# Kernel optimization log

Hardware: AMD Instinct MI355X
Metric: run time of the kernel (lower is better)

The kernel has to match this reference:

```python
import jax, jax.numpy as jnp
import numpy as np

N_NODES = 10000
N_GRAPHS = 64
IN_DIM = 256
HID = 256
N_CLASSES = 10
N_EDGES = 320000


def _gcn_conv(x, W, b, src, dst):
    # PyG GCNConv: h = x @ W; add self-loops (weight 1); symmetric norm D^-1/2 (A+I) D^-1/2; aggregate; + b
    N = x.shape[0]
    h = x @ W  # [N, H]
    loops = jnp.arange(N, dtype=src.dtype)
    s = jnp.concatenate([src, loops])
    d = jnp.concatenate([dst, loops])
    w = jnp.ones(s.shape[0], dtype=x.dtype)
    deg = jax.ops.segment_sum(w, d, num_segments=N)
    dinv = jnp.where(deg > 0, jax.lax.rsqrt(jnp.maximum(deg, 1.0)), 0.0)
    norm = dinv[s] * dinv[d]  # [E+N]
    msg = h[s] * norm[:, None]  # gather + scale
    out = jax.ops.segment_sum(msg, d, num_segments=N)  # scatter-add
    return out + b


def setup_inputs() -> dict:
    key = jax.random.key(0)
    ks = jax.random.split(key, 12)
    x = jax.random.normal(ks[0], (N_NODES, IN_DIM), dtype=jnp.float32)
    edge_index = jax.random.randint(ks[1], (2, N_EDGES), 0, N_NODES, dtype=jnp.int64)
    batch = jnp.sort(jax.random.randint(ks[2], (N_NODES,), 0, N_GRAPHS, dtype=jnp.int64))
    g = 1.0 / np.sqrt(IN_DIM)
    W1 = jax.random.uniform(ks[3], (IN_DIM, HID), jnp.float32, -g, g)
    b1 = jnp.zeros((HID,), jnp.float32)
    gh = 1.0 / np.sqrt(HID)
    W2 = jax.random.uniform(ks[4], (HID, HID), jnp.float32, -gh, gh)
    b2 = jnp.zeros((HID,), jnp.float32)
    W3 = jax.random.uniform(ks[5], (HID, HID), jnp.float32, -gh, gh)
    b3 = jnp.zeros((HID,), jnp.float32)
    Wlin = jax.random.uniform(ks[6], (HID, N_CLASSES), jnp.float32, -gh, gh)
    blin = jax.random.uniform(ks[7], (N_CLASSES,), jnp.float32, -gh, gh)
    return {"x": x, "W1": W1, "b1": b1, "W2": W2, "b2": b2, "W3": W3, "b3": b3,
            "Wlin": Wlin, "blin": blin, "edge_index": edge_index, "batch": batch}


def reference(x, W1, b1, W2, b2, W3, b3, Wlin, blin, edge_index, batch):
    src, dst = edge_index[0], edge_index[1]
    h = jax.nn.relu(_gcn_conv(x, W1, b1, src, dst))
    h = jax.nn.relu(_gcn_conv(h, W2, b2, src, dst))
    h = jax.nn.relu(_gcn_conv(h, W3, b3, src, dst))
    # global mean pool over graphs (dropout is identity in eval mode)
    sums = jax.ops.segment_sum(h, batch, num_segments=N_GRAPHS)  # [G, H]
    cnts = jax.ops.segment_sum(jnp.ones((h.shape[0],), h.dtype), batch, num_segments=N_GRAPHS)
    pooled = sums / jnp.maximum(cnts, 1.0)[:, None]
    logits = pooled @ Wlin + blin
    return jax.nn.log_softmax(logits, axis=-1)
```

## Files before the change

kernel.cpp:

```cpp
#include <hip/hip_runtime.h>
#include <hip/hip_bf16.h>
#include <math.h>

#define HIDDEN 256
#define NCLS 10

typedef __attribute__((ext_vector_type(8))) short short8;
typedef __attribute__((ext_vector_type(4))) float f32x4;

static __device__ __forceinline__ float bf16lo(unsigned u) {
    return __uint_as_float((u & 0xffffu) << 16);
}
static __device__ __forceinline__ float bf16hi(unsigned u) {
    return __uint_as_float(u & 0xffff0000u);
}
static __device__ __forceinline__ unsigned short f2bf(float f) {
    unsigned x = __float_as_uint(f);
    x += 0x7fffu + ((x >> 16) & 1u);
    return (unsigned short)(x >> 16);
}
static __device__ __forceinline__ unsigned pack2(float lo, float hi) {
    return (unsigned)f2bf(lo) | ((unsigned)f2bf(hi) << 16);
}

static __device__ __forceinline__ void fma8(float* acc, uint4 u, float w) {
    acc[0] = fmaf(bf16lo(u.x), w, acc[0]);
    acc[1] = fmaf(bf16hi(u.x), w, acc[1]);
    acc[2] = fmaf(bf16lo(u.y), w, acc[2]);
    acc[3] = fmaf(bf16hi(u.y), w, acc[3]);
    acc[4] = fmaf(bf16lo(u.z), w, acc[4]);
    acc[5] = fmaf(bf16hi(u.z), w, acc[5]);
    acc[6] = fmaf(bf16lo(u.w), w, acc[6]);
    acc[7] = fmaf(bf16hi(u.w), w, acc[7]);
}

__global__ __launch_bounds__(256) void k_count_prep(const int* __restrict__ dst,
                                                    int* __restrict__ ecnt, int E,
                                                    const float* __restrict__ x,
                                                    unsigned* __restrict__ x16,
                                                    const float* __restrict__ W1,
                                                    const float* __restrict__ W2,
                                                    const float* __restrict__ W3,
                                                    short8* __restrict__ P1,
                                                    short8* __restrict__ P2,
                                                    short8* __restrict__ P3,
                                                    int n4, int nbCount, int nb_cvt) {
    const int b = blockIdx.x;
    if (b < nbCount) {
        int e = b * 256 + threadIdx.x;
        if (e < E) atomicAdd(&ecnt[dst[e]], 1);
    } else if (b < nbCount + nb_cvt) {
        int i = (b - nbCount) * 256 + threadIdx.x;
        if (i < n4) {
            float4 v = reinterpret_cast<const float4*>(x)[i];
            uint2 o;
            o.x = pack2(v.x, v.y);
            o.y = pack2(v.z, v.w);
            reinterpret_cast<uint2*>(x16)[i] = o;
        }
    } else {
        int pb = b - nbCount - nb_cvt;
        int which = pb >> 5;
        int id = (pb & 31) * 256 + threadIdx.x;
        const float* W = (which == 0) ? W1 : (which == 1) ? W2 : W3;
        short8* P = (which == 0) ? P1 : (which == 1) ? P2 : P3;
        int l = id & 63;
        int tt = (id >> 6) & 15;
        int s = id >> 10;
        int col = tt * 16 + (l & 15);
        int k0 = s * 32 + (l >> 4) * 8;
        short8 v;
#pragma unroll
        for (int j = 0; j < 8; ++j)
            v[j] = (short)f2bf(W[(size_t)(k0 + j) * HIDDEN + col]);
        P[id] = v;
    }
}

__global__ __launch_bounds__(1024) void k_scan(const int* __restrict__ ecnt,
                                               int* __restrict__ rowstart,
                                               int* __restrict__ cursor,
                                               float* __restrict__ dinv, int N, int E) {
    __shared__ int sums[1024];
    int t = threadIdx.x;
    const int CH = (N + 1023) / 1024;
    int base = t * CH;
    int local = 0;
    for (int i = 0; i < CH; ++i) {
        int idx = base + i;
        if (idx < N) local += ecnt[idx];
    }
    sums[t] = local;
    __syncthreads();
    for (int off = 1; off < 1024; off <<= 1) {
        int v = (t >= off) ? sums[t - off] : 0;
        __syncthreads();
        sums[t] += v;
        __syncthreads();
    }
    int run = (t == 0) ? 0 : sums[t - 1];
    for (int i = 0; i < CH; ++i) {
        int idx = base + i;
        if (idx < N) {
            rowstart[idx] = run;
            cursor[idx] = run;
            dinv[idx] = rsqrtf((float)(ecnt[idx] + 1));
            run += ecnt[idx];
        }
    }
    if (t == 0) rowstart[N] = E;
}

static __device__ __forceinline__ void gemm_body(const unsigned short* __restrict__ A,
                                                 const short8* __restrict__ P,
                                                 unsigned short* __restrict__ C,
                                                 int bx, int by, int tid) {
    const int l = tid & 63;
    const int w = tid >> 6;
    const int g = l >> 4;
    const int r = l & 15;
    const int mwave = bx * 64 + w * 16;
    const int nb = by * 4;

    f32x4 acc[4] = {};
    const unsigned short* arow = A + (size_t)(mwave + r) * HIDDEN;

#pragma unroll
    for (int s = 0; s < 8; ++s) {
        short8 a = *reinterpret_cast<const short8*>(arow + s * 32 + g * 8);
#pragma unroll
        for (int f = 0; f < 4; ++f) {
            short8 bfrag = P[(s * 16 + nb + f) * 64 + l];
            acc[f] = __builtin_amdgcn_mfma_f32_16x16x32_bf16(a, bfrag, acc[f], 0, 0, 0);
        }
    }
#pragma unroll
    for (int f = 0; f < 4; ++f) {
        int col = by * 64 + f * 16 + r;
#pragma unroll
        for (int q = 0; q < 4; ++q) {
            int row = mwave + g * 4 + q;
            C[(size_t)row * HIDDEN + col] = f2bf(acc[f][q]);
        }
    }
}

__global__ __launch_bounds__(256) void k_gemm(const unsigned short* __restrict__ A,
                                              const short8* __restrict__ P,
                                              unsigned short* __restrict__ C) {
    gemm_body(A, P, C, blockIdx.x, blockIdx.y, threadIdx.x);
}

__global__ __launch_bounds__(256) void k_fill_gemm1(const int* __restrict__ src,
                                                    const int* __restrict__ dst,
                                                    const float* __restrict__ dinv,
                                                    int* __restrict__ cursor,
                                                    uint2* __restrict__ csr, int E,
                                                    const unsigned short* __restrict__ A,
                                                    const short8* __restrict__ P,
                                                    unsigned short* __restrict__ C,
                                                    int nbFill) {
    const int b = blockIdx.x;
    if (b < nbFill) {
        int e = b * 256 + threadIdx.x;
        if (e < E) {
            int d = dst[e];
            int s = src[e];
            int pos = atomicAdd(&cursor[d], 1);
            uint2 ent;
            ent.x = (unsigned)s;
            ent.y = __float_as_uint(dinv[s] * dinv[d]);
            csr[pos] = ent;
        }
    } else {
        int gb = b - nbFill;
        gemm_body(A, P, C, gb >> 2, gb & 3, threadIdx.x);
    }
}

__global__ __launch_bounds__(256) void k_agg(const unsigned* __restrict__ H,
                                             const uint2* __restrict__ csr,
                                             const int* __restrict__ rowstart,
                                             const float* __restrict__ dinv,
                                             const float* __restrict__ bias,
                                             unsigned* __restrict__ out, int N) {
    const int n = blockIdx.x * 4 + (threadIdx.x >> 6);
    if (n >= N) return;
    const int l = threadIdx.x & 63;
    const int q = l & 31;
    const int h = l >> 5;
    const uint4* __restrict__ H4 = reinterpret_cast<const uint4*>(H);

    float acc[8] = {0.f, 0.f, 0.f, 0.f, 0.f, 0.f, 0.f, 0.f};
    if (h == 0) {
        const float di = dinv[n];
        fma8(acc, H4[(size_t)n * 32 + q], di * di);
    }

    const int base = rowstart[n];
    const int e1   = rowstart[n + 1];
    const int nfull = (e1 - base) >> 3;
    const uint2* cp = csr + base + 4 * h;

    if (nfull > 0) {
        uint2 dA0 = cp[0], dA1 = cp[1], dA2 = cp[2], dA3 = cp[3];
        uint4 rA0 = H4[(size_t)dA0.x * 32 + q];
        uint4 rA1 = H4[(size_t)dA1.x * 32 + q];
        uint4 rA2 = H4[(size_t)dA2.x * 32 + q];
        uint4 rA3 = H4[(size_t)dA3.x * 32 + q];
        uint2 dB0 = cp[8], dB1 = cp[9], dB2 = cp[10], dB3 = cp[11];
        for (int it = 0; it + 1 < nfull; ++it) {
            cp += 8;
            uint4 rB0 = H4[(size_t)dB0.x * 32 + q];
            uint4 rB1 = H4[(size_t)dB1.x * 32 + q];
            uint4 rB2 = H4[(size_t)dB2.x * 32 + q];
            uint4 rB3 = H4[(size_t)dB3.x * 32 + q];
            uint2 dC0 = cp[8], dC1 = cp[9], dC2 = cp[10], dC3 = cp[11];
            fma8(acc, rA0, __uint_as_float(dA0.y));
            fma8(acc, rA1, __uint_as_float(dA1.y));
            fma8(acc, rA2, __uint_as_float(dA2.y));
            fma8(acc, rA3, __uint_as_float(dA3.y));
            dA0 = dB0; dA1 = dB1; dA2 = dB2; dA3 = dB3;
            dB0 = dC0; dB1 = dC1; dB2 = dC2; dB3 = dC3;
            rA0 = rB0; rA1 = rB1; rA2 = rB2; rA3 = rB3;
        }
        fma8(acc, rA0, __uint_as_float(dA0.y));
        fma8(acc, rA1, __uint_as_float(dA1.y));
        fma8(acc, rA2, __uint_as_float(dA2.y));
        fma8(acc, rA3, __uint_as_float(dA3.y));
    }
    for (int e = base + 8 * nfull + h; e < e1; e += 2) {
        uint2 ed = csr[e];
        fma8(acc, H4[(size_t)ed.x * 32 + q], __uint_as_float(ed.y));
    }

#pragma unroll
    for (int j = 0; j < 8; ++j) acc[j] += __shfl_xor(acc[j], 32);

    if (h == 0) {
        const float4* __restrict__ b4 = reinterpret_cast<const float4*>(bias);
        float4 ba = b4[q * 2];
        float4 bb = b4[q * 2 + 1];
        uint4 o;
        o.x = pack2(fmaxf(acc[0] + ba.x, 0.f), fmaxf(acc[1] + ba.y, 0.f));
        o.y = pack2(fmaxf(acc[2] + ba.z, 0.f), fmaxf(acc[3] + ba.w, 0.f));
        o.z = pack2(fmaxf(acc[4] + bb.x, 0.f), fmaxf(acc[5] + bb.y, 0.f));
        o.w = pack2(fmaxf(acc[6] + bb.z, 0.f), fmaxf(acc[7] + bb.w, 0.f));
        reinterpret_cast<uint4*>(out)[(size_t)n * 32 + q] = o;
    }
}

__device__ __forceinline__ int lower_bound_i(const int* a, int n, int val) {
    int lo = 0, hi = n;
    while (lo < hi) {
        int mid = (lo + hi) >> 1;
        if (a[mid] < val) lo = mid + 1; else hi = mid;
    }
    return lo;
}

__global__ __launch_bounds__(128) void k_pool_part(const unsigned* __restrict__ H,
                                                   const int* __restrict__ batch,
                                                   float* __restrict__ partial, int N) {
    const int g = blockIdx.x;
    const int s = blockIdx.y;
    const int p = threadIdx.x;
    const int lo = lower_bound_i(batch, N, g);
    const int hi = lower_bound_i(batch, N, g + 1);
    float sx = 0.f, sy = 0.f;
    for (int n = lo + s; n < hi; n += 8) {
        unsigned u = H[(size_t)n * 128 + p];
        sx += bf16lo(u);
        sy += bf16hi(u);
    }
    float2 v; v.x = sx; v.y = sy;
    reinterpret_cast<float2*>(partial)[(size_t)(g * 8 + s) * 128 + p] = v;
}

__global__ __launch_bounds__(256) void k_cls(const float* __restrict__ partial,
                                             const int* __restrict__ batch,
                                             const float* __restrict__ Wlin,
                                             const float* __restrict__ blin,
                                             float* __restrict__ out, int N) {
    __shared__ float part[NCLS][HIDDEN];
    const int g = blockIdx.x;
    const int t = threadIdx.x;
    const int lo = lower_bound_i(batch, N, g);
    const int hi = lower_bound_i(batch, N, g + 1);
    float p = 0.f;
#pragma unroll
    for (int s = 0; s < 8; ++s) p += partial[(size_t)(g * 8 + s) * HIDDEN + t];
    p /= fmaxf((float)(hi - lo), 1.f);
#pragma unroll
    for (int c = 0; c < NCLS; ++c) part[c][t] = p * Wlin[(size_t)t * NCLS + c];
    __syncthreads();
    for (int off = 128; off >= 1; off >>= 1) {
        if (t < off) {
#pragma unroll
            for (int c = 0; c < NCLS; ++c) part[c][t] += part[c][t + off];
        }
        __syncthreads();
    }
    if (t == 0) {
        float lg[NCLS];
        float m = -INFINITY;
#pragma unroll
        for (int c = 0; c < NCLS; ++c) {
            lg[c] = part[c][0] + blin[c];
            m = fmaxf(m, lg[c]);
        }
        float se = 0.f;
#pragma unroll
        for (int c = 0; c < NCLS; ++c) se += expf(lg[c] - m);
        float lse = m + logf(se);
#pragma unroll
        for (int c = 0; c < NCLS; ++c) out[(size_t)g * NCLS + c] = lg[c] - lse;
    }
}


extern "C" void kernel_launch(void* const* d_in, const int* in_sizes, int n_in,
                              void* d_out, int out_size, void* d_ws, size_t ws_size,
                              hipStream_t stream) {
    const float* x    = (const float*)d_in[0];
    const float* W1   = (const float*)d_in[1];
    const float* b1   = (const float*)d_in[2];
    const float* W2   = (const float*)d_in[3];
    const float* b2   = (const float*)d_in[4];
    const float* W3   = (const float*)d_in[5];
    const float* b3   = (const float*)d_in[6];
    const float* Wlin = (const float*)d_in[7];
    const float* blin = (const float*)d_in[8];
    const int*   eidx = (const int*)d_in[9];
    const int*   batch= (const int*)d_in[10];
    float* out = (float*)d_out;

    const int N = in_sizes[0] / HIDDEN;
    const int E = in_sizes[9] / 2;
    const int G = out_size / NCLS;
    const int Mp = (N + 63) & ~63;

    const int* src = eidx;
    const int* dst = eidx + E;

    char* base = (char*)d_ws;
    size_t off = 0;
    auto alloc = [&](size_t bytes) -> void* {
        void* p = base + off;
        off = (off + bytes + 255) & ~(size_t)255;
        return p;
    };
    int*      ecnt     = (int*)     alloc((size_t)N * sizeof(int));
    int*      cursor   = (int*)     alloc((size_t)N * sizeof(int));
    float*    dinv     = (float*)   alloc((size_t)N * sizeof(float));
    int*      rowstart = (int*)     alloc((size_t)(N + 1) * sizeof(int));
    uint2*    csr      = (uint2*)   alloc((size_t)(E + 16) * sizeof(uint2));
    unsigned* x16      = (unsigned*)alloc((size_t)Mp * 128 * sizeof(unsigned));
    unsigned* hA       = (unsigned*)alloc((size_t)Mp * 128 * sizeof(unsigned));
    unsigned* hB       = (unsigned*)alloc((size_t)Mp * 128 * sizeof(unsigned));
    short8*   Wp1      = (short8*)  alloc((size_t)8192 * sizeof(short8));
    short8*   Wp2      = (short8*)  alloc((size_t)8192 * sizeof(short8));
    short8*   Wp3      = (short8*)  alloc((size_t)8192 * sizeof(short8));
    float*    partial  = (float*)   alloc((size_t)G * 8 * HIDDEN * sizeof(float));
    (void)ws_size;

    const int nbCount = (E + 255) / 256;
    const int n4 = N * HIDDEN / 4;
    const int nb_cvt = (n4 + 255) / 256;
    hipMemsetAsync(ecnt, 0, (size_t)N * sizeof(int), stream);
    k_count_prep<<<nbCount + nb_cvt + 96, 256, 0, stream>>>(
        dst, ecnt, E, x, x16, W1, W2, W3, Wp1, Wp2, Wp3, n4, nbCount, nb_cvt);
    k_scan<<<1, 1024, 0, stream>>>(ecnt, rowstart, cursor, dinv, N, E);

    const int nbFill = (E + 255) / 256;
    const int gemmBlocks = (Mp / 64) * 4;
    k_fill_gemm1<<<nbFill + gemmBlocks, 256, 0, stream>>>(
        src, dst, dinv, cursor, csr, E,
        (const unsigned short*)x16, Wp1, (unsigned short*)hA, nbFill);

    const dim3 ggrid(Mp / 64, 4);
    const int agg_blocks = (N + 3) / 4;
    k_agg <<<agg_blocks, 256, 0, stream>>>(hA, csr, rowstart, dinv, b1, hB, N);
    k_gemm<<<ggrid, 256, 0, stream>>>((const unsigned short*)hB, Wp2, (unsigned short*)hA);
    k_agg <<<agg_blocks, 256, 0, stream>>>(hA, csr, rowstart, dinv, b2, hB, N);
    k_gemm<<<ggrid, 256, 0, stream>>>((const unsigned short*)hB, Wp3, (unsigned short*)hA);
    k_agg <<<agg_blocks, 256, 0, stream>>>(hA, csr, rowstart, dinv, b3, hB, N);
    k_pool_part<<<dim3(G, 8), 128, 0, stream>>>(hB, batch, partial, N);
    k_cls <<<G, 256, 0, stream>>>(partial, batch, Wlin, blin, out, N);
}
```

Measured before the change: 166.2 us.

## Split feature matrices into two column halves so aggregation covers one half per pass

Node feature buffers are stored as two contiguous 128-column halves instead of row-major 256 columns. The aggregation kernel gains a second grid dimension, one per half, so each wave gathers 256-byte rows with one dword per lane. It also pipelines 8 edges at a time, double-buffered, in place of the previous split-wave uint4 scheme that needed a cross-half shuffle. The goal is a smaller working set per pass for better L2 reuse and no shuffle reduction, at the cost of reading CSR indices twice and using narrower per-lane loads. The GEMM, pool and classifier indexing are updated to match the new layout.

Measured after the change: 204.4 us. 1.23x slower.

```diff
diff --git a/kernel.cpp b/kernel.cpp
--- a/kernel.cpp
+++ b/kernel.cpp
@@ -9,7 +9,7 @@
 typedef __attribute__((ext_vector_type(4))) float f32x4;
 
 static __device__ __forceinline__ float bf16lo(unsigned u) {
-    return __uint_as_float((u & 0xffffu) << 16);
+    return __uint_as_float(u << 16);
 }
 static __device__ __forceinline__ float bf16hi(unsigned u) {
     return __uint_as_float(u & 0xffff0000u);
@@ -23,16 +23,6 @@
     return (unsigned)f2bf(lo) | ((unsigned)f2bf(hi) << 16);
 }
 
-static __device__ __forceinline__ void fma8(float* acc, uint4 u, float w) {
-    acc[0] = fmaf(bf16lo(u.x), w, acc[0]);
-    acc[1] = fmaf(bf16hi(u.x), w, acc[1]);
-    acc[2] = fmaf(bf16lo(u.y), w, acc[2]);
-    acc[3] = fmaf(bf16hi(u.y), w, acc[3]);
-    acc[4] = fmaf(bf16lo(u.z), w, acc[4]);
-    acc[5] = fmaf(bf16hi(u.z), w, acc[5]);
-    acc[6] = fmaf(bf16lo(u.w), w, acc[6]);
-    acc[7] = fmaf(bf16hi(u.w), w, acc[7]);
-}
 
 __global__ __launch_bounds__(256) void k_count_prep(const int* __restrict__ dst,
                                                     int* __restrict__ ecnt, int E,
@@ -44,7 +34,8 @@
                                                     short8* __restrict__ P1,
                                                     short8* __restrict__ P2,
                                                     short8* __restrict__ P3,
-                                                    int n4, int nbCount, int nb_cvt) {
+                                                    int n4, int nbCount, int nb_cvt,
+                                                    int Mp) {
     const int b = blockIdx.x;
     if (b < nbCount) {
         int e = b * 256 + threadIdx.x;
@@ -56,7 +47,11 @@
             uint2 o;
             o.x = pack2(v.x, v.y);
             o.y = pack2(v.z, v.w);
-            reinterpret_cast<uint2*>(x16)[i] = o;
+            int row = i >> 6;
+            int c4  = i & 63;
+            int half = c4 >> 5;
+            size_t idx = (size_t)half * Mp * 32 + (size_t)row * 32 + (c4 & 31);
+            reinterpret_cast<uint2*>(x16)[idx] = o;
         }
     } else {
         int pb = b - nbCount - nb_cvt;
@@ -114,7 +109,7 @@
 static __device__ __forceinline__ void gemm_body(const unsigned short* __restrict__ A,
                                                  const short8* __restrict__ P,
                                                  unsigned short* __restrict__ C,
-                                                 int bx, int by, int tid) {
+                                                 int bx, int by, int tid, int Mp) {
     const int l = tid & 63;
     const int w = tid >> 6;
     const int g = l >> 4;
@@ -123,11 +118,13 @@
     const int nb = by * 4;
 
     f32x4 acc[4] = {};
-    const unsigned short* arow = A + (size_t)(mwave + r) * HIDDEN;
+    const unsigned short* arow0 = A + (size_t)(mwave + r) * 128 + g * 8;
+    const unsigned short* arow1 = arow0 + (size_t)Mp * 128;
 
 #pragma unroll
     for (int s = 0; s < 8; ++s) {
-        short8 a = *reinterpret_cast<const short8*>(arow + s * 32 + g * 8);
+        const unsigned short* ap = (s < 4) ? arow0 : arow1;
+        short8 a = *reinterpret_cast<const short8*>(ap + (s & 3) * 32);
 #pragma unroll
         for (int f = 0; f < 4; ++f) {
             short8 bfrag = P[(s * 16 + nb + f) * 64 + l];
@@ -137,18 +134,19 @@
 #pragma unroll
     for (int f = 0; f < 4; ++f) {
         int col = by * 64 + f * 16 + r;
+        unsigned short* cb = C + (size_t)(col >> 7) * Mp * 128 + (col & 127);
 #pragma unroll
         for (int q = 0; q < 4; ++q) {
             int row = mwave + g * 4 + q;
-            C[(size_t)row * HIDDEN + col] = f2bf(acc[f][q]);
+            cb[(size_t)row * 128] = f2bf(acc[f][q]);
         }
     }
 }
 
 __global__ __launch_bounds__(256) void k_gemm(const unsigned short* __restrict__ A,
                                               const short8* __restrict__ P,
-                                              unsigned short* __restrict__ C) {
-    gemm_body(A, P, C, blockIdx.x, blockIdx.y, threadIdx.x);
+                                              unsigned short* __restrict__ C, int Mp) {
+    gemm_body(A, P, C, blockIdx.x, blockIdx.y, threadIdx.x, Mp);
 }
 
 __global__ __launch_bounds__(256) void k_fill_gemm1(const int* __restrict__ src,
@@ -159,7 +157,7 @@
                                                     const unsigned short* __restrict__ A,
                                                     const short8* __restrict__ P,
                                                     unsigned short* __restrict__ C,
-                                                    int nbFill) {
+                                                    int nbFill, int Mp) {
     const int b = blockIdx.x;
     if (b < nbFill) {
         int e = b * 256 + threadIdx.x;
@@ -174,7 +172,7 @@
         }
     } else {
         int gb = b - nbFill;
-        gemm_body(A, P, C, gb >> 2, gb & 3, threadIdx.x);
+        gemm_body(A, P, C, gb >> 2, gb & 3, threadIdx.x, Mp);
     }
 }
 
@@ -183,71 +181,103 @@
                                              const int* __restrict__ rowstart,
                                              const float* __restrict__ dinv,
                                              const float* __restrict__ bias,
-                                             unsigned* __restrict__ out, int N) {
+                                             unsigned* __restrict__ out, int N, int Mp) {
     const int n = blockIdx.x * 4 + (threadIdx.x >> 6);
     if (n >= N) return;
+    const int p = blockIdx.y;
     const int l = threadIdx.x & 63;
-    const int q = l & 31;
-    const int h = l >> 5;
-    const uint4* __restrict__ H4 = reinterpret_cast<const uint4*>(H);
-
-    float acc[8] = {0.f, 0.f, 0.f, 0.f, 0.f, 0.f, 0.f, 0.f};
-    if (h == 0) {
+    const unsigned* __restrict__ Hh = H + (size_t)p * Mp * 64;
+
+    float ax, ay;
+    {
         const float di = dinv[n];
-        fma8(acc, H4[(size_t)n * 32 + q], di * di);
+        unsigned u = Hh[(size_t)n * 64 + l];
+        ax = bf16lo(u) * (di * di);
+        ay = bf16hi(u) * (di * di);
     }
 
     const int base = rowstart[n];
     const int e1   = rowstart[n + 1];
     const int nfull = (e1 - base) >> 3;
-    const uint2* cp = csr + base + 4 * h;
+    const uint2* cp = csr + base;
 
     if (nfull > 0) {
-        uint2 dA0 = cp[0], dA1 = cp[1], dA2 = cp[2], dA3 = cp[3];
-        uint4 rA0 = H4[(size_t)dA0.x * 32 + q];
-        uint4 rA1 = H4[(size_t)dA1.x * 32 + q];
-        uint4 rA2 = H4[(size_t)dA2.x * 32 + q];
-        uint4 rA3 = H4[(size_t)dA3.x * 32 + q];
-        uint2 dB0 = cp[8], dB1 = cp[9], dB2 = cp[10], dB3 = cp[11];
-        for (int it = 0; it + 1 < nfull; ++it) {
+        uint2 d1[8];
+        unsigned r0[8], r1[8];
+        float w0[8], w1[8];
+        {
+            uint2 d0[8];
+#pragma unroll
+            for (int j = 0; j < 8; ++j) d0[j] = cp[j];
+#pragma unroll
+            for (int j = 0; j < 8; ++j) {
+                r0[j] = Hh[(size_t)d0[j].x * 64 + l];
+                w0[j] = __uint_as_float(d0[j].y);
+            }
+#pragma unroll
+            for (int j = 0; j < 8; ++j) d1[j] = cp[8 + j];
+        }
+        int it = 0;
+        for (; it + 2 < nfull; it += 2) {
+#pragma unroll
+            for (int j = 0; j < 8; ++j) r1[j] = Hh[(size_t)d1[j].x * 64 + l];
+#pragma unroll
+            for (int j = 0; j < 8; ++j) w1[j] = __uint_as_float(d1[j].y);
+#pragma unroll
+            for (int j = 0; j < 8; ++j) d1[j] = cp[16 + j];
+#pragma unroll
+            for (int j = 0; j < 8; ++j) {
+                ax = fmaf(bf16lo(r0[j]), w0[j], ax);
+                ay = fmaf(bf16hi(r0[j]), w0[j], ay);
+            }
             cp += 8;
-            uint4 rB0 = H4[(size_t)dB0.x * 32 + q];
-            uint4 rB1 = H4[(size_t)dB1.x * 32 + q];
-            uint4 rB2 = H4[(size_t)dB2.x * 32 + q];
-            uint4 rB3 = H4[(size_t)dB3.x * 32 + q];
-            uint2 dC0 = cp[8], dC1 = cp[9], dC2 = cp[10], dC3 = cp[11];
-            fma8(acc, rA0, __uint_as_float(dA0.y));
-            fma8(acc, rA1, __uint_as_float(dA1.y));
-            fma8(acc, rA2, __uint_as_float(dA2.y));
-            fma8(acc, rA3, __uint_as_float(dA3.y));
-            dA0 = dB0; dA1 = dB1; dA2 = dB2; dA3 = dB3;
-            dB0 = dC0; dB1 = dC1; dB2 = dC2; dB3 = dC3;
-            rA0 = rB0; rA1 = rB1; rA2 = rB2; rA3 = rB3;
-        }
-        fma8(acc, rA0, __uint_as_float(dA0.y));
-        fma8(acc, rA1, __uint_as_float(dA1.y));
-        fma8(acc, rA2, __uint_as_float(dA2.y));
-        fma8(acc, rA3, __uint_as_float(dA3.y));
-    }
-    for (int e = base + 8 * nfull + h; e < e1; e += 2) {
+#pragma unroll
+            for (int j = 0; j < 8; ++j) r0[j] = Hh[(size_t)d1[j].x * 64 + l];
+#pragma unroll
+            for (int j = 0; j < 8; ++j) w0[j] = __uint_as_float(d1[j].y);
+#pragma unroll
+            for (int j = 0; j < 8; ++j) d1[j] = cp[16 + j];
+#pragma unroll
+            for (int j = 0; j < 8; ++j) {
+                ax = fmaf(bf16lo(r1[j]), w1[j], ax);
+                ay = fmaf(bf16hi(r1[j]), w1[j], ay);
+            }
+            cp += 8;
+        }
+        if (nfull - it == 2) {
+#pragma unroll
+            for (int j = 0; j < 8; ++j) r1[j] = Hh[(size_t)d1[j].x * 64 + l];
+#pragma unroll
+            for (int j = 0; j < 8; ++j) w1[j] = __uint_as_float(d1[j].y);
+#pragma unroll
+            for (int j = 0; j < 8; ++j) {
+                ax = fmaf(bf16lo(r0[j]), w0[j], ax);
+                ay = fmaf(bf16hi(r0[j]), w0[j], ay);
+            }
+#pragma unroll
+            for (int j = 0; j < 8; ++j) {
+                ax = fmaf(bf16lo(r1[j]), w1[j], ax);
+                ay = fmaf(bf16hi(r1[j]), w1[j], ay);
+            }
+        } else {
+#pragma unroll
+            for (int j = 0; j < 8; ++j) {
+                ax = fmaf(bf16lo(r0[j]), w0[j], ax);
+                ay = fmaf(bf16hi(r0[j]), w0[j], ay);
+            }
+        }
+    }
+    for (int e = base + 8 * nfull; e < e1; ++e) {
         uint2 ed = csr[e];
-        fma8(acc, H4[(size_t)ed.x * 32 + q], __uint_as_float(ed.y));
-    }
-
-#pragma unroll
-    for (int j = 0; j < 8; ++j) acc[j] += __shfl_xor(acc[j], 32);
-
-    if (h == 0) {
-        const float4* __restrict__ b4 = reinterpret_cast<const float4*>(bias);
-        float4 ba = b4[q * 2];
-        float4 bb = b4[q * 2 + 1];
-        uint4 o;
-        o.x = pack2(fmaxf(acc[0] + ba.x, 0.f), fmaxf(acc[1] + ba.y, 0.f));
-        o.y = pack2(fmaxf(acc[2] + ba.z, 0.f), fmaxf(acc[3] + ba.w, 0.f));
-        o.z = pack2(fmaxf(acc[4] + bb.x, 0.f), fmaxf(acc[5] + bb.y, 0.f));
-        o.w = pack2(fmaxf(acc[6] + bb.z, 0.f), fmaxf(acc[7] + bb.w, 0.f));
-        reinterpret_cast<uint4*>(out)[(size_t)n * 32 + q] = o;
-    }
+        unsigned u = Hh[(size_t)ed.x * 64 + l];
+        float w = __uint_as_float(ed.y);
+        ax = fmaf(bf16lo(u), w, ax);
+        ay = fmaf(bf16hi(u), w, ay);
+    }
+
+    const float2 bv = reinterpret_cast<const float2*>(bias)[p * 64 + l];
+    out[(size_t)p * Mp * 64 + (size_t)n * 64 + l] =
+        pack2(fmaxf(ax + bv.x, 0.f), fmaxf(ay + bv.y, 0.f));
 }
 
 __device__ __forceinline__ int lower_bound_i(const int* a, int n, int val) {
@@ -261,15 +291,18 @@
 
 __global__ __launch_bounds__(128) void k_pool_part(const unsigned* __restrict__ H,
                                                    const int* __restrict__ batch,
-                                                   float* __restrict__ partial, int N) {
+                                                   float* __restrict__ partial,
+                                                   int N, int Mp) {
     const int g = blockIdx.x;
     const int s = blockIdx.y;
     const int p = threadIdx.x;
+    const unsigned* __restrict__ Hh = H + (size_t)(p >> 6) * Mp * 64;
+    const int c = p & 63;
     const int lo = lower_bound_i(batch, N, g);
     const int hi = lower_bound_i(batch, N, g + 1);
     float sx = 0.f, sy = 0.f;
     for (int n = lo + s; n < hi; n += 8) {
-        unsigned u = H[(size_t)n * 128 + p];
+        unsigned u = Hh[(size_t)n * 64 + c];
         sx += bf16lo(u);
         sy += bf16hi(u);
     }
@@ -285,6 +318,7 @@
     __shared__ float part[NCLS][HIDDEN];
     const int g = blockIdx.x;
     const int t = threadIdx.x;
+    const int ch = ((t >> 1) >> 6) * 128 + 2 * ((t >> 1) & 63) + (t & 1);
     const int lo = lower_bound_i(batch, N, g);
     const int hi = lower_bound_i(batch, N, g + 1);
     float p = 0.f;
@@ -292,7 +326,7 @@
     for (int s = 0; s < 8; ++s) p += partial[(size_t)(g * 8 + s) * HIDDEN + t];
     p /= fmaxf((float)(hi - lo), 1.f);
 #pragma unroll
-    for (int c = 0; c < NCLS; ++c) part[c][t] = p * Wlin[(size_t)t * NCLS + c];
+    for (int c = 0; c < NCLS; ++c) part[c][t] = p * Wlin[(size_t)ch * NCLS + c];
     __syncthreads();
     for (int off = 128; off >= 1; off >>= 1) {
         if (t < off) {
@@ -369,22 +403,22 @@
     const int nb_cvt = (n4 + 255) / 256;
     hipMemsetAsync(ecnt, 0, (size_t)N * sizeof(int), stream);
     k_count_prep<<<nbCount + nb_cvt + 96, 256, 0, stream>>>(
-        dst, ecnt, E, x, x16, W1, W2, W3, Wp1, Wp2, Wp3, n4, nbCount, nb_cvt);
+        dst, ecnt, E, x, x16, W1, W2, W3, Wp1, Wp2, Wp3, n4, nbCount, nb_cvt, Mp);
     k_scan<<<1, 1024, 0, stream>>>(ecnt, rowstart, cursor, dinv, N, E);
 
     const int nbFill = (E + 255) / 256;
     const int gemmBlocks = (Mp / 64) * 4;
     k_fill_gemm1<<<nbFill + gemmBlocks, 256, 0, stream>>>(
         src, dst, dinv, cursor, csr, E,
-        (const unsigned short*)x16, Wp1, (unsigned short*)hA, nbFill);
+        (const unsigned short*)x16, Wp1, (unsigned short*)hA, nbFill, Mp);
 
     const dim3 ggrid(Mp / 64, 4);
-    const int agg_blocks = (N + 3) / 4;
-    k_agg <<<agg_blocks, 256, 0, stream>>>(hA, csr, rowstart, dinv, b1, hB, N);
-    k_gemm<<<ggrid, 256, 0, stream>>>((const unsigned short*)hB, Wp2, (unsigned short*)hA);
-    k_agg <<<agg_blocks, 256, 0, stream>>>(hA, csr, rowstart, dinv, b2, hB, N);
-    k_gemm<<<ggrid, 256, 0, stream>>>((const unsigned short*)hB, Wp3, (unsigned short*)hA);
-    k_agg <<<agg_blocks, 256, 0, stream>>>(hA, csr, rowstart, dinv, b3, hB, N);
-    k_pool_part<<<dim3(G, 8), 128, 0, stream>>>(hB, batch, partial, N);
+    const dim3 agrid((N + 3) / 4, 2);
+    k_agg <<<agrid, 256, 0, stream>>>(hA, csr, rowstart, dinv, b1, hB, N, Mp);
+    k_gemm<<<ggrid, 256, 0, stream>>>((const unsigned short*)hB, Wp2, (unsigned short*)hA, Mp);
+    k_agg <<<agrid, 256, 0, stream>>>(hA, csr, rowstart, dinv, b2, hB, N, Mp);
+    k_gemm<<<ggrid, 256, 0, stream>>>((const unsigned short*)hB, Wp3, (unsigned short*)hA, Mp);
+    k_agg <<<agrid, 256, 0, stream>>>(hA, csr, rowstart, dinv, b3, hB, N, Mp);
+    k_pool_part<<<dim3(G, 8), 128, 0, stream>>>(hB, batch, partial, N, Mp);
     k_cls <<<G, 256, 0, stream>>>(partial, batch, Wlin, blin, out, N);
 }
```

## Split aggregation feature dimension across two blocks, four edge streams per wave

Applied to the files above, without the earlier changes.

The aggregation kernel now launches a 2D grid. Each block column handles half of the 256 hidden features, with 16 lanes per row-half, and each wave processes four interleaved edge streams instead of two. The change doubles the number of waves to raise memory-level parallelism for the irregular row gathers, and adds an extra shuffle reduction step. It also uses nontemporal loads for the CSR entries and nontemporal stores for the output, and pads the CSR buffer for the deeper prefetch. In exchange, each CSR entry is read twice (once per feature half) and each gather covers only 256 bytes per edge row per wave.

New measurement: 193.3 us. 16.3% more time.

```diff
diff --git a/kernel.cpp b/kernel.cpp
--- a/kernel.cpp
+++ b/kernel.cpp
@@ -7,9 +7,10 @@
 
 typedef __attribute__((ext_vector_type(8))) short short8;
 typedef __attribute__((ext_vector_type(4))) float f32x4;
+typedef __attribute__((ext_vector_type(4))) unsigned u32x4;
 
 static __device__ __forceinline__ float bf16lo(unsigned u) {
-    return __uint_as_float((u & 0xffffu) << 16);
+    return __uint_as_float(u << 16);
 }
 static __device__ __forceinline__ float bf16hi(unsigned u) {
     return __uint_as_float(u & 0xffff0000u);
@@ -186,67 +187,74 @@
                                              unsigned* __restrict__ out, int N) {
     const int n = blockIdx.x * 4 + (threadIdx.x >> 6);
     if (n >= N) return;
+    const int p = blockIdx.y;
     const int l = threadIdx.x & 63;
-    const int q = l & 31;
-    const int h = l >> 5;
+    const int qa = l >> 4;
+    const int c  = l & 15;
+    const int hoff = p * 16 + c;
     const uint4* __restrict__ H4 = reinterpret_cast<const uint4*>(H);
 
     float acc[8] = {0.f, 0.f, 0.f, 0.f, 0.f, 0.f, 0.f, 0.f};
-    if (h == 0) {
+    if (qa == 0) {
         const float di = dinv[n];
-        fma8(acc, H4[(size_t)n * 32 + q], di * di);
+        fma8(acc, H4[(size_t)n * 32 + hoff], di * di);
     }
 
     const int base = rowstart[n];
     const int e1   = rowstart[n + 1];
-    const int nfull = (e1 - base) >> 3;
-    const uint2* cp = csr + base + 4 * h;
+    const int nfull = (e1 - base) >> 4;
+    const unsigned long long* cp =
+        reinterpret_cast<const unsigned long long*>(csr) + base + qa * 4;
 
     if (nfull > 0) {
-        uint2 dA0 = cp[0], dA1 = cp[1], dA2 = cp[2], dA3 = cp[3];
-        uint4 rA0 = H4[(size_t)dA0.x * 32 + q];
-        uint4 rA1 = H4[(size_t)dA1.x * 32 + q];
-        uint4 rA2 = H4[(size_t)dA2.x * 32 + q];
-        uint4 rA3 = H4[(size_t)dA3.x * 32 + q];
-        uint2 dB0 = cp[8], dB1 = cp[9], dB2 = cp[10], dB3 = cp[11];
+        unsigned long long dA[4], dB[4];
+        uint4 rA[4];
+#pragma unroll
+        for (int j = 0; j < 4; ++j) dA[j] = __builtin_nontemporal_load(cp + j);
+#pragma unroll
+        for (int j = 0; j < 4; ++j) rA[j] = H4[(size_t)(unsigned)dA[j] * 32 + hoff];
+#pragma unroll
+        for (int j = 0; j < 4; ++j) dB[j] = __builtin_nontemporal_load(cp + 16 + j);
+
         for (int it = 0; it + 1 < nfull; ++it) {
-            cp += 8;
-            uint4 rB0 = H4[(size_t)dB0.x * 32 + q];
-            uint4 rB1 = H4[(size_t)dB1.x * 32 + q];
-            uint4 rB2 = H4[(size_t)dB2.x * 32 + q];
-            uint4 rB3 = H4[(size_t)dB3.x * 32 + q];
-            uint2 dC0 = cp[8], dC1 = cp[9], dC2 = cp[10], dC3 = cp[11];
-            fma8(acc, rA0, __uint_as_float(dA0.y));
-            fma8(acc, rA1, __uint_as_float(dA1.y));
-            fma8(acc, rA2, __uint_as_float(dA2.y));
-            fma8(acc, rA3, __uint_as_float(dA3.y));
-            dA0 = dB0; dA1 = dB1; dA2 = dB2; dA3 = dB3;
-            dB0 = dC0; dB1 = dC1; dB2 = dC2; dB3 = dC3;
-            rA0 = rB0; rA1 = rB1; rA2 = rB2; rA3 = rB3;
-        }
-        fma8(acc, rA0, __uint_as_float(dA0.y));
-        fma8(acc, rA1, __uint_as_float(dA1.y));
-        fma8(acc, rA2, __uint_as_float(dA2.y));
-        fma8(acc, rA3, __uint_as_float(dA3.y));
-    }
-    for (int e = base + 8 * nfull + h; e < e1; e += 2) {
+            cp += 16;
+            uint4 rB[4];
+#pragma unroll
+            for (int j = 0; j < 4; ++j) rB[j] = H4[(size_t)(unsigned)dB[j] * 32 + hoff];
+            unsigned long long dC[4];
+#pragma unroll
+            for (int j = 0; j < 4; ++j) dC[j] = __builtin_nontemporal_load(cp + 16 + j);
+#pragma unroll
+            for (int j = 0; j < 4; ++j)
+                fma8(acc, rA[j], __uint_as_float((unsigned)(dA[j] >> 32)));
+#pragma unroll
+            for (int j = 0; j < 4; ++j) { dA[j] = dB[j]; dB[j] = dC[j]; rA[j] = rB[j]; }
+        }
+#pragma unroll
+        for (int j = 0; j < 4; ++j)
+            fma8(acc, rA[j], __uint_as_float((unsigned)(dA[j] >> 32)));
+    }
+    for (int e = base + 16 * nfull + qa; e < e1; e += 4) {
         uint2 ed = csr[e];
-        fma8(acc, H4[(size_t)ed.x * 32 + q], __uint_as_float(ed.y));
-    }
-
-#pragma unroll
-    for (int j = 0; j < 8; ++j) acc[j] += __shfl_xor(acc[j], 32);
-
-    if (h == 0) {
+        fma8(acc, H4[(size_t)ed.x * 32 + hoff], __uint_as_float(ed.y));
+    }
+
+#pragma unroll
+    for (int j = 0; j < 8; ++j) {
+        acc[j] += __shfl_xor(acc[j], 16);
+        acc[j] += __shfl_xor(acc[j], 32);
+    }
+
+    if (qa == 0) {
         const float4* __restrict__ b4 = reinterpret_cast<const float4*>(bias);
-        float4 ba = b4[q * 2];
-        float4 bb = b4[q * 2 + 1];
-        uint4 o;
+        float4 ba = b4[hoff * 2];
+        float4 bb = b4[hoff * 2 + 1];
+        u32x4 o;
         o.x = pack2(fmaxf(acc[0] + ba.x, 0.f), fmaxf(acc[1] + ba.y, 0.f));
         o.y = pack2(fmaxf(acc[2] + ba.z, 0.f), fmaxf(acc[3] + ba.w, 0.f));
         o.z = pack2(fmaxf(acc[4] + bb.x, 0.f), fmaxf(acc[5] + bb.y, 0.f));
         o.w = pack2(fmaxf(acc[6] + bb.z, 0.f), fmaxf(acc[7] + bb.w, 0.f));
-        reinterpret_cast<uint4*>(out)[(size_t)n * 32 + q] = o;
+        __builtin_nontemporal_store(o, reinterpret_cast<u32x4*>(out) + (size_t)n * 32 + hoff);
     }
 }
 
@@ -354,7 +362,7 @@
     int*      cursor   = (int*)     alloc((size_t)N * sizeof(int));
     float*    dinv     = (float*)   alloc((size_t)N * sizeof(float));
     int*      rowstart = (int*)     alloc((size_t)(N + 1) * sizeof(int));
-    uint2*    csr      = (uint2*)   alloc((size_t)(E + 16) * sizeof(uint2));
+    uint2*    csr      = (uint2*)   alloc((size_t)(E + 32) * sizeof(uint2));
     unsigned* x16      = (unsigned*)alloc((size_t)Mp * 128 * sizeof(unsigned));
     unsigned* hA       = (unsigned*)alloc((size_t)Mp * 128 * sizeof(unsigned));
     unsigned* hB       = (unsigned*)alloc((size_t)Mp * 128 * sizeof(unsigned));
@@ -367,7 +375,7 @@
     const int nbCount = (E + 255) / 256;
     const int n4 = N * HIDDEN / 4;
     const int nb_cvt = (n4 + 255) / 256;
-    hipMemsetAsync(ecnt, 0, (size_t)N * sizeof(int), stream);
+    (void)hipMemsetAsync(ecnt, 0, (size_t)N * sizeof(int), stream);
     k_count_prep<<<nbCount + nb_cvt + 96, 256, 0, stream>>>(
         dst, ecnt, E, x, x16, W1, W2, W3, Wp1, Wp2, Wp3, n4, nbCount, nb_cvt);
     k_scan<<<1, 1024, 0, stream>>>(ecnt, rowstart, cursor, dinv, N, E);
@@ -379,12 +387,12 @@
         (const unsigned short*)x16, Wp1, (unsigned short*)hA, nbFill);
 
     const dim3 ggrid(Mp / 64, 4);
-    const int agg_blocks = (N + 3) / 4;
-    k_agg <<<agg_blocks, 256, 0, stream>>>(hA, csr, rowstart, dinv, b1, hB, N);
+    const dim3 agrid((N + 3) / 4, 2);
+    k_agg <<<agrid, 256, 0, stream>>>(hA, csr, rowstart, dinv, b1, hB, N);
     k_gemm<<<ggrid, 256, 0, stream>>>((const unsigned short*)hB, Wp2, (unsigned short*)hA);
-    k_agg <<<agg_blocks, 256, 0, stream>>>(hA, csr, rowstart, dinv, b2, hB, N);
+    k_agg <<<agrid, 256, 0, stream>>>(hA, csr, rowstart, dinv, b2, hB, N);
     k_gemm<<<ggrid, 256, 0, stream>>>((const unsigned short*)hB, Wp3, (unsigned short*)hA);
-    k_agg <<<agg_blocks, 256, 0, stream>>>(hA, csr, rowstart, dinv, b3, hB, N);
+    k_agg <<<agrid, 256, 0, stream>>>(hA, csr, rowstart, dinv, b3, hB, N);
     k_pool_part<<<dim3(G, 8), 128, 0, stream>>>(hB, batch, partial, N);
     k_cls <<<G, 256, 0, stream>>>(partial, batch, Wlin, blin, out, N);
 }
```
